# Kernel tuning notes

Hardware: AMD Instinct MI355X
Metric: run time of the kernel (lower is better)

Reference implementation:

```python
import jax, jax.numpy as jnp
import numpy as np

B, L, D = 2, 2048, 1024
H, G = 16, 2            # num_heads, num_kv_groups
HPG = H // G            # heads per kv group = 8
DQK, DV = 128, 128      # qk_head_dim, v_head_dim (head_dim=64, ratios=2.0)


def setup_inputs() -> dict:
    key = jax.random.key(0)
    ks = jax.random.split(key, 12)

    def xavier(k, shape, scale=1.0):
        fan_in, fan_out = shape[0], shape[1]
        lim = np.sqrt(6.0 / (fan_in + fan_out))
        return jax.random.uniform(k, shape, jnp.float32, -lim, lim) * scale

    return {
        "in_q": jax.random.normal(ks[0], (B, L, D), jnp.float32),
        "in_k": jax.random.normal(ks[1], (B, L, D), jnp.float32),
        "in_v": jax.random.normal(ks[2], (B, L, D), jnp.float32),
        # weights stored as [in, out] (transpose of torch Linear); qk_init_scale=0.5
        "Wq": xavier(ks[3], (D, H * DQK), 0.5),
        "bq": jnp.zeros((H * DQK,), jnp.float32),
        "Wk": xavier(ks[4], (D, G * DQK), 0.5),
        "bk": jnp.zeros((G * DQK,), jnp.float32),
        "Wv": xavier(ks[5], (D, G * DV)),
        "bv": jnp.zeros((G * DV,), jnp.float32),
        "Wo": xavier(ks[6], (H * DV, D)),
        "bo": jnp.zeros((D,), jnp.float32),
        "q_extra_scale": jnp.ones((1,), jnp.float32),
    }


def reference(in_q, in_k, in_v, Wq, bq, Wk, bk, Wv, bv, Wo, bo, q_extra_scale):
    # fused projections
    q = (in_q @ Wq + bq) * q_extra_scale              # [B,L,H*DQK]
    k = in_k @ Wk + bk                                 # [B,L,G*DQK]
    v = in_v @ Wv + bv                                 # [B,L,G*DV]

    # reshape: keep GQA group structure instead of materializing repeat_interleave
    q = q.reshape(B, L, G, HPG, DQK)                   # heads grouped: head h = g*HPG + m
    k = k.reshape(B, L, G, DQK)
    v = v.reshape(B, L, G, DV)

    scale = 1.0 / np.sqrt(DQK)
    # scores: [B,G,HPG,L_q,L_kv]
    scores = jnp.einsum("bsgmd,btgd->bgmst", q, k) * scale
    causal = jnp.tril(jnp.ones((L, L), bool))          # is_causal=True
    scores = jnp.where(causal, scores, jnp.finfo(scores.dtype).min)
    attn = jax.nn.softmax(scores, axis=-1)
    ctx = jnp.einsum("bgmst,btgd->bsgmd", attn, v)     # [B,L,G,HPG,DV]
    ctx = ctx.reshape(B, L, H * DV)
    return ctx @ Wo + bo                               # [B,L,D]
```

## Files before the change

### kernel.cpp

```cpp
#include <hip/hip_runtime.h>


typedef __bf16 bf16;
typedef __bf16 bf16x8 __attribute__((ext_vector_type(8)));
typedef __bf16 bf16x4 __attribute__((ext_vector_type(4)));
typedef float f32x4 __attribute__((ext_vector_type(4)));
typedef float f32x16 __attribute__((ext_vector_type(16)));
typedef float float4v __attribute__((ext_vector_type(4)));

#define MFMA_BF16(a, b, c) __builtin_amdgcn_mfma_f32_16x16x32_bf16((a), (b), (c), 0, 0, 0)
#define MFMA32(a, b, c)    __builtin_amdgcn_mfma_f32_32x32x16_bf16((a), (b), (c), 0, 0, 0)

static constexpr int Bz = 2, Lz = 2048, Dz = 1024;
static constexpr int Hz = 16, Gz = 2;
static constexpr int DQKz = 128, DVz = 128;

__device__ __forceinline__ void async_copy16(const bf16* g, bf16* l) {
    __builtin_amdgcn_global_load_lds(
        (const __attribute__((address_space(1))) unsigned int*)g,
        (__attribute__((address_space(3))) unsigned int*)l, 16, 0, 0);
}

__device__ __forceinline__ unsigned cvt_pk_bf16(float lo, float hi) {
    unsigned r;
    asm("v_cvt_pk_bf16_f32 %0, %1, %2" : "=v"(r) : "v"(lo), "v"(hi));
    return r;
}

__global__ __launch_bounds__(256) void prep(
    const float* __restrict__ q, const float* __restrict__ k,
    const float* __restrict__ v, bf16* __restrict__ dq,
    bf16* __restrict__ dk, bf16* __restrict__ dv,
    const float* __restrict__ Wq, const float* __restrict__ Wk,
    const float* __restrict__ Wv, const float* __restrict__ Wo,
    bf16* __restrict__ WqT, bf16* __restrict__ WkT,
    bf16* __restrict__ WvT, bf16* __restrict__ WoT)
{
    int bid = blockIdx.x;
    if (bid < 6144) {
        const float* s = bid < 2048 ? q : (bid < 4096 ? k : v);
        bf16* d = bid < 2048 ? dq : (bid < 4096 ? dk : dv);
        int i = (bid & 2047) * 2048 + threadIdx.x * 8;
        float4v a = *(const float4v*)(s + i);
        float4v b = *(const float4v*)(s + i + 4);
        bf16x8 o;
        #pragma unroll
        for (int j = 0; j < 4; ++j) { o[j] = (bf16)a[j]; o[j + 4] = (bf16)b[j]; }
        *(bf16x8*)(d + i) = o;
        return;
    }
    bid -= 6144;
    const float* W; bf16* WT; int K, N;
    if (bid < 2048)      { W = Wq; WT = WqT; K = 1024; N = 2048; }
    else if (bid < 2304) { W = Wk; WT = WkT; K = 1024; N = 256;  bid -= 2048; }
    else if (bid < 2560) { W = Wv; WT = WvT; K = 1024; N = 256;  bid -= 2304; }
    else                 { W = Wo; WT = WoT; K = 2048; N = 1024; bid -= 2560; }
    int tiles_n = N >> 5;
    int n0 = (bid % tiles_n) * 32, k0 = (bid / tiles_n) * 32;

    __shared__ bf16 t[32][33];
    int tx = threadIdx.x & 31, ty = threadIdx.x >> 5;
    #pragma unroll
    for (int i = 0; i < 4; ++i)
        t[ty + i * 8][tx] = (bf16)W[(size_t)(k0 + ty + i * 8) * N + n0 + tx];
    __syncthreads();
    #pragma unroll
    for (int i = 0; i < 4; ++i)
        WT[(size_t)(n0 + ty + i * 8) * K + k0 + tx] = t[tx][ty + i * 8];
}

template <typename TC>
__device__ __forceinline__ void gemm_tile(
    const bf16* __restrict__ A, const bf16* __restrict__ BT,
    const float* __restrict__ bias, float scale, TC* __restrict__ C,
    int M, int N, int K, int m0, int n0, bool trans_out,
    bf16 (&As)[2][128 * 64], bf16 (&Bs)[2][128 * 64])
{
    const int tid  = threadIdx.x;
    const int wave = tid >> 6;
    const int lane = tid & 63;
    const int quad = lane >> 4;
    const int l16  = lane & 15;
    const int sw   = l16 & 7;
    const int wm = wave >> 2, wn = wave & 3;

    f32x4 acc[4][2] = {};

    auto stage = [&](int k0, int buf) {
        #pragma unroll
        for (int s = 0; s < 2; ++s) {
            int i = s * 512 + tid;
            int row = i >> 3, c = (i & 7) ^ (row & 7);
            async_copy16(A + (size_t)(m0 + row) * K + k0 + c * 8, &As[buf][i * 8]);
        }
        #pragma unroll
        for (int s = 0; s < 2; ++s) {
            int i = s * 512 + tid;
            int row = i >> 3, c = (i & 7) ^ (row & 7);
            async_copy16(BT + (size_t)(n0 + row) * K + k0 + c * 8, &Bs[buf][i * 8]);
        }
    };

    stage(0, 0);
    int cur = 0;
    for (int k0 = 0; k0 < K; k0 += 64) {
        __syncthreads();
        if (k0 + 64 < K) stage(k0 + 64, cur ^ 1);

        #pragma unroll
        for (int ks = 0; ks < 2; ++ks) {
            bf16x8 af[4], bfv[2];
            #pragma unroll
            for (int mt = 0; mt < 4; ++mt)
                af[mt] = *(const bf16x8*)(&As[cur][((wm * 64 + mt * 16 + l16) * 8
                                                    + ((ks * 4 + quad) ^ sw)) * 8]);
            #pragma unroll
            for (int nt = 0; nt < 2; ++nt)
                bfv[nt] = *(const bf16x8*)(&Bs[cur][((wn * 32 + nt * 16 + l16) * 8
                                                     + ((ks * 4 + quad) ^ sw)) * 8]);
            #pragma unroll
            for (int mt = 0; mt < 4; ++mt)
                #pragma unroll
                for (int nt = 0; nt < 2; ++nt)
                    acc[mt][nt] = MFMA_BF16(af[mt], bfv[nt], acc[mt][nt]);
        }
        cur ^= 1;
    }

    #pragma unroll
    for (int nt = 0; nt < 2; ++nt) {
        int col = n0 + wn * 32 + nt * 16 + l16;
        float bv = bias[col];
        #pragma unroll
        for (int mt = 0; mt < 4; ++mt) {
            int row = m0 + wm * 64 + mt * 16 + quad * 4;
            if (trans_out) {
                struct V4 { TC v[4]; } o;
                #pragma unroll
                for (int r = 0; r < 4; ++r)
                    o.v[r] = (TC)((acc[mt][nt][r] + bv) * scale);
                *(V4*)(&C[(size_t)col * M + row]) = o;
            } else {
                #pragma unroll
                for (int r = 0; r < 4; ++r)
                    C[(size_t)(row + r) * N + col] =
                        (TC)((acc[mt][nt][r] + bv) * scale);
            }
        }
    }
}

__global__ __launch_bounds__(512, 4) void proj_qkv(
    const bf16* __restrict__ aq, const bf16* __restrict__ ak,
    const bf16* __restrict__ av, const bf16* __restrict__ WqT,
    const bf16* __restrict__ WkT, const bf16* __restrict__ WvT,
    const float* __restrict__ bq, const float* __restrict__ bk,
    const float* __restrict__ bv, const float* __restrict__ qsc,
    bf16* __restrict__ Qw, bf16* __restrict__ Kw, bf16* __restrict__ VwT)
{
    __shared__ bf16 As[2][128 * 64];
    __shared__ bf16 Bs[2][128 * 64];
    int bid = blockIdx.x;
    if (bid < 512) {
        float scale = qsc[0] * 0.08838834764831845f * 1.4426950408889634f;
        gemm_tile<bf16>(aq, WqT, bq, scale, Qw, 4096, 2048, 1024,
                        (bid >> 4) * 128, (bid & 15) * 128, false, As, Bs);
    } else if (bid < 576) {
        int b2 = bid - 512;
        gemm_tile<bf16>(ak, WkT, bk, 1.0f, Kw, 4096, 256, 1024,
                        (b2 >> 1) * 128, (b2 & 1) * 128, false, As, Bs);
    } else {
        int b2 = bid - 576;
        gemm_tile<bf16>(av, WvT, bv, 1.0f, VwT, 4096, 256, 1024,
                        (b2 >> 1) * 128, (b2 & 1) * 128, true, As, Bs);
    }
}

__global__ __launch_bounds__(512, 4) void proj_o(
    const bf16* __restrict__ Cw, const bf16* __restrict__ WoT,
    const float* __restrict__ bo, float* __restrict__ out)
{
    __shared__ bf16 As[2][128 * 64];
    __shared__ bf16 Bs[2][128 * 64];
    gemm_tile<float>(Cw, WoT, bo, 1.0f, out, 4096, 1024, 2048,
                     (blockIdx.x >> 3) * 128, (blockIdx.x & 7) * 128,
                     false, As, Bs);
}

__global__ __launch_bounds__(256, 2) void attn_fused(
    const bf16* __restrict__ Q,
    const bf16* __restrict__ Kp,
    const bf16* __restrict__ VT,
    bf16* __restrict__ ctx)
{
    __shared__ bf16 Kb[2][64 * 128];
    __shared__ bf16 Vb[2][128 * 64];

    const int tid  = threadIdx.x;
    const int wave = tid >> 6;
    const int lane = tid & 63;
    const int hi   = lane >> 5;
    const int l31  = lane & 31;
    const int s7   = l31 & 7;
    const int wq   = wave >> 1;
    const int kvw  = wave & 1;

    const int h = blockIdx.y;
    const int b = blockIdx.z;
    const int g = h >> 3;

    const bf16* kgbase = Kp + (size_t)(b * Lz) * (Gz * DQKz) + g * DQKz;
    const bf16* vgbase = VT + (size_t)(g * DVz) * (Bz * Lz) + b * Lz;

    int kgo[4], vgo[4], ldso[4];
    #pragma unroll
    for (int s = 0; s < 4; ++s) {
        int i = s * 256 + tid;
        ldso[s] = i * 8;
        int key = i >> 4, ck = (i & 15) ^ (key & 7);
        kgo[s] = key * (Gz * DQKz) + ck * 8;
        int dvr = i >> 3, cv = (i & 7) ^ (dvr & 7);
        vgo[s] = dvr * (Bz * Lz) + cv * 8;
    }
    auto stage = [&](int kt, int buf) {
        const bf16* kb = kgbase + (size_t)(kt * 64) * (Gz * DQKz);
        const bf16* vb = vgbase + kt * 64;
        #pragma unroll
        for (int s = 0; s < 4; ++s) async_copy16(kb + kgo[s], &Kb[buf][ldso[s]]);
        #pragma unroll
        for (int s = 0; s < 4; ++s) async_copy16(vb + vgo[s], &Vb[buf][ldso[s]]);
    };

    int koff[8];
    #pragma unroll
    for (int ks = 0; ks < 8; ++ks)
        koff[ks] = ((kvw * 32 + l31) * 16 + ((ks * 2 + hi) ^ s7)) * 8;
    int voff[4][2];
    #pragma unroll
    for (int dt = 0; dt < 4; ++dt)
        #pragma unroll
        for (int kss = 0; kss < 2; ++kss)
            voff[dt][kss] = ((dt * 32 + l31) * 8
                             + ((kvw * 4 + kss * 2 + hi) ^ s7)) * 8;

    for (int pass = 0; pass < 2; ++pass) {
        const int qt  = pass == 0 ? (31 - (int)blockIdx.x) : (int)blockIdx.x;
        const int q0  = qt * 64;
        const int nkt = qt + 1;
        const int qrow = q0 + wq * 32 + l31;

        bf16x8 qf[8];
        {
            const bf16* qbase = Q + (size_t)(b * Lz + qrow) * (Hz * DQKz) + h * DQKz;
            #pragma unroll
            for (int s = 0; s < 8; ++s)
                qf[s] = *(const bf16x8*)(qbase + s * 16 + hi * 8);
        }

        f32x16 oacc0 = {}, oacc1 = {}, oacc2 = {}, oacc3 = {};
        float lsum = 0.0f;

        if (pass) __syncthreads();
        stage(0, 0);
        int cur = 0;

        for (int kt = 0; kt < nkt; ++kt) {
            __syncthreads();
            if (kt + 1 < nkt) stage(kt + 1, cur ^ 1);

            const bf16* kcur = Kb[cur];
            const bf16* vcur = Vb[cur];

            f32x16 sacc = {};
            #pragma unroll
            for (int ks = 0; ks < 8; ++ks) {
                bf16x8 kf = *(const bf16x8*)(kcur + koff[ks]);
                sacc = MFMA32(kf, qf[ks], sacc);
            }

            float pv[16];
            if (kt == nkt - 1) {
                #pragma unroll
                for (int r = 0; r < 16; ++r) {
                    int key = kvw * 32 + (r & 3) + 8 * (r >> 2) + 4 * hi;
                    pv[r] = (key > wq * 32 + l31) ? 0.0f
                                                  : exp2f(sacc[r] - 8.0f);
                }
            } else {
                #pragma unroll
                for (int r = 0; r < 16; ++r)
                    pv[r] = exp2f(sacc[r] - 8.0f);
            }
            lsum += ((pv[0] + pv[1]) + (pv[2] + pv[3]))
                  + ((pv[4] + pv[5]) + (pv[6] + pv[7]))
                  + ((pv[8] + pv[9]) + (pv[10] + pv[11]))
                  + ((pv[12] + pv[13]) + (pv[14] + pv[15]));

            unsigned c0 = cvt_pk_bf16(pv[0],  pv[1]);
            unsigned c1 = cvt_pk_bf16(pv[2],  pv[3]);
            unsigned c2 = cvt_pk_bf16(pv[4],  pv[5]);
            unsigned c3 = cvt_pk_bf16(pv[6],  pv[7]);
            unsigned c4 = cvt_pk_bf16(pv[8],  pv[9]);
            unsigned c5 = cvt_pk_bf16(pv[10], pv[11]);
            unsigned c6 = cvt_pk_bf16(pv[12], pv[13]);
            unsigned c7 = cvt_pk_bf16(pv[14], pv[15]);
            asm("v_permlane32_swap_b32 %0, %1" : "+v"(c0), "+v"(c2));
            asm("v_permlane32_swap_b32 %0, %1" : "+v"(c1), "+v"(c3));
            asm("v_permlane32_swap_b32 %0, %1" : "+v"(c4), "+v"(c6));
            asm("v_permlane32_swap_b32 %0, %1" : "+v"(c5), "+v"(c7));
            union { unsigned u[4]; bf16x8 v; } p0 = {{c0, c1, c2, c3}};
            union { unsigned u[4]; bf16x8 v; } p1 = {{c4, c5, c6, c7}};

            {
                bf16x8 vf;
                vf = *(const bf16x8*)(vcur + voff[0][0]); oacc0 = MFMA32(vf, p0.v, oacc0);
                vf = *(const bf16x8*)(vcur + voff[0][1]); oacc0 = MFMA32(vf, p1.v, oacc0);
                vf = *(const bf16x8*)(vcur + voff[1][0]); oacc1 = MFMA32(vf, p0.v, oacc1);
                vf = *(const bf16x8*)(vcur + voff[1][1]); oacc1 = MFMA32(vf, p1.v, oacc1);
                vf = *(const bf16x8*)(vcur + voff[2][0]); oacc2 = MFMA32(vf, p0.v, oacc2);
                vf = *(const bf16x8*)(vcur + voff[2][1]); oacc2 = MFMA32(vf, p1.v, oacc2);
                vf = *(const bf16x8*)(vcur + voff[3][0]); oacc3 = MFMA32(vf, p0.v, oacc3);
                vf = *(const bf16x8*)(vcur + voff[3][1]); oacc3 = MFMA32(vf, p1.v, oacc3);
            }
            cur ^= 1;
        }

        lsum += __shfl_xor(lsum, 32);

        float* E0 = (float*)Kb;
        float* E1 = (float*)Vb;
        float* LS = (float*)Vb + 6000;
        __syncthreads();

        auto store_partial = [&](f32x16 v, float* E) {
            #pragma unroll
            for (int j = 0; j < 4; ++j) {
                f32x4 v4 = { v[4 * j], v[4 * j + 1], v[4 * j + 2], v[4 * j + 3] };
                *(f32x4*)&E[(wave * 64 + lane) * 20 + 4 * j] = v4;
            }
        };
        if (kvw == 0) { store_partial(oacc2, E0); store_partial(oacc3, E1); }
        else          { store_partial(oacc0, E0); store_partial(oacc1, E1); }
        if (lane < 32) LS[wave * 32 + lane] = lsum;
        __syncthreads();
        lsum += LS[(wave ^ 1) * 32 + l31];
        const float inv = 1.0f / lsum;

        bf16* cbase = ctx + (size_t)(b * Lz + qrow) * (Hz * DVz) + h * DVz;
        auto finalize = [&](f32x16 v, float* E, int dt) {
            #pragma unroll
            for (int j = 0; j < 4; ++j) {
                f32x4 p4 = *(const f32x4*)&E[((wave ^ 1) * 64 + lane) * 20 + 4 * j];
                bf16x4 o4;
                #pragma unroll
                for (int r = 0; r < 4; ++r)
                    o4[r] = (bf16)((v[4 * j + r] + p4[r]) * inv);
                *(bf16x4*)&cbase[dt * 32 + j * 8 + hi * 4] = o4;
            }
        };
        if (kvw == 0) { finalize(oacc0, E0, 0); finalize(oacc1, E1, 1); }
        else          { finalize(oacc2, E0, 2); finalize(oacc3, E1, 3); }
    }
}

extern "C" void kernel_launch(void* const* d_in, const int* in_sizes, int n_in,
                              void* d_out, int out_size, void* d_ws, size_t ws_size,
                              hipStream_t stream)
{
    (void)in_sizes; (void)n_in; (void)out_size; (void)ws_size;

    const float* in_q = (const float*)d_in[0];
    const float* in_k = (const float*)d_in[1];
    const float* in_v = (const float*)d_in[2];
    const float* Wq   = (const float*)d_in[3];
    const float* bq   = (const float*)d_in[4];
    const float* Wk   = (const float*)d_in[5];
    const float* bk   = (const float*)d_in[6];
    const float* Wv   = (const float*)d_in[7];
    const float* bv   = (const float*)d_in[8];
    const float* Wo   = (const float*)d_in[9];
    const float* bo   = (const float*)d_in[10];
    const float* qsc  = (const float*)d_in[11];
    float* out = (float*)d_out;

    const int M = Bz * Lz;
    const int NQ = Hz * DQKz;
    const int NKV = Gz * DQKz;

    bf16* aq  = (bf16*)d_ws;
    bf16* WqT = aq  + (size_t)M * Dz;
    bf16* WkT = WqT + (size_t)NQ * Dz;
    bf16* WvT = WkT + (size_t)NKV * Dz;
    bf16* WoT = WvT + (size_t)NKV * Dz;
    bf16* Qw  = WoT + (size_t)Dz * NQ;
    bf16* Kw  = Qw  + (size_t)M * NQ;
    bf16* VwT = Kw  + (size_t)M * NKV;
    bf16* Cw  = VwT + (size_t)NKV * M;
    bf16* ak  = Cw;
    bf16* av  = Cw + (size_t)M * Dz;

    prep<<<dim3(10752), dim3(256), 0, stream>>>(
        in_q, in_k, in_v, aq, ak, av, Wq, Wk, Wv, Wo, WqT, WkT, WvT, WoT);

    proj_qkv<<<dim3(640), dim3(512), 0, stream>>>(
        aq, ak, av, WqT, WkT, WvT, bq, bk, bv, qsc, Qw, Kw, VwT);

    attn_fused<<<dim3(Lz / 128, Hz, Bz), dim3(256), 0, stream>>>(Qw, Kw, VwT, Cw);

    proj_o<<<dim3(256), dim3(512), 0, stream>>>(Cw, WoT, bo, out);
}
```

Baseline: 246.0 us.

## Single-buffer K, one q-tile per block, raise attention occupancy

The attention kernel no longer processes two paired q-tiles per block. It launches one block per 64-row q-tile (32 blocks along x) and relies on scheduling to balance the causal work. K is now single-buffered in shared memory while V stays double-buffered, cutting LDS from 64KB to 48KB so three blocks can fit per CU (launch bounds 3). An extra barrier separates the QK MFMAs from the next K/V prefetch, and s_setprio raises wave priority around the MFMA sections. The cost is less K prefetch overlap, since the K load now waits until the QK step finishes, plus one more barrier per iteration and a loss of the explicit load balancing the tile pairing provided.

```diff
diff --git a/kernel.cpp b/kernel.cpp
--- a/kernel.cpp
+++ b/kernel.cpp
@@ -187,14 +187,13 @@
                      false, As, Bs);
 }
 
-__global__ __launch_bounds__(256, 2) void attn_fused(
+__global__ __launch_bounds__(256, 3) void attn_fused(
     const bf16* __restrict__ Q,
     const bf16* __restrict__ Kp,
     const bf16* __restrict__ VT,
     bf16* __restrict__ ctx)
 {
-    __shared__ bf16 Kb[2][64 * 128];
-    __shared__ bf16 Vb[2][128 * 64];
+    __shared__ bf16 smem[24576];
 
     const int tid  = threadIdx.x;
     const int wave = tid >> 6;
@@ -222,13 +221,16 @@
         int dvr = i >> 3, cv = (i & 7) ^ (dvr & 7);
         vgo[s] = dvr * (Bz * Lz) + cv * 8;
     }
-    auto stage = [&](int kt, int buf) {
+    auto stage_K = [&](int kt) {
         const bf16* kb = kgbase + (size_t)(kt * 64) * (Gz * DQKz);
+        #pragma unroll
+        for (int s = 0; s < 4; ++s) async_copy16(kb + kgo[s], smem + ldso[s]);
+    };
+    auto stage_V = [&](int kt, int buf) {
         const bf16* vb = vgbase + kt * 64;
         #pragma unroll
-        for (int s = 0; s < 4; ++s) async_copy16(kb + kgo[s], &Kb[buf][ldso[s]]);
-        #pragma unroll
-        for (int s = 0; s < 4; ++s) async_copy16(vb + vgo[s], &Vb[buf][ldso[s]]);
+        for (int s = 0; s < 4; ++s)
+            async_copy16(vb + vgo[s], smem + 8192 + buf * 8192 + ldso[s]);
     };
 
     int koff[8];
@@ -243,124 +245,131 @@
             voff[dt][kss] = ((dt * 32 + l31) * 8
                              + ((kvw * 4 + kss * 2 + hi) ^ s7)) * 8;
 
-    for (int pass = 0; pass < 2; ++pass) {
-        const int qt  = pass == 0 ? (31 - (int)blockIdx.x) : (int)blockIdx.x;
-        const int q0  = qt * 64;
-        const int nkt = qt + 1;
-        const int qrow = q0 + wq * 32 + l31;
-
-        bf16x8 qf[8];
+    const int qt  = 31 - (int)blockIdx.x;
+    const int q0  = qt * 64;
+    const int nkt = qt + 1;
+    const int qrow = q0 + wq * 32 + l31;
+
+    bf16x8 qf[8];
+    {
+        const bf16* qbase = Q + (size_t)(b * Lz + qrow) * (Hz * DQKz) + h * DQKz;
+        #pragma unroll
+        for (int s = 0; s < 8; ++s)
+            qf[s] = *(const bf16x8*)(qbase + s * 16 + hi * 8);
+    }
+
+    f32x16 oacc0 = {}, oacc1 = {}, oacc2 = {}, oacc3 = {};
+    float lsum = 0.0f;
+
+    stage_K(0);
+    stage_V(0, 0);
+    int cur = 0;
+
+    for (int kt = 0; kt < nkt; ++kt) {
+        __syncthreads();
+
+        const bf16* vcur = smem + 8192 + cur * 8192;
+
+        f32x16 sacc = {};
+        __builtin_amdgcn_s_setprio(1);
+        #pragma unroll
+        for (int ks = 0; ks < 8; ++ks) {
+            bf16x8 kf = *(const bf16x8*)(smem + koff[ks]);
+            sacc = MFMA32(kf, qf[ks], sacc);
+        }
+        __builtin_amdgcn_s_setprio(0);
+
+        __syncthreads();
+        if (kt + 1 < nkt) {
+            stage_K(kt + 1);
+            stage_V(kt + 1, cur ^ 1);
+        }
+
+        float pv[16];
+        if (kt == nkt - 1) {
+            #pragma unroll
+            for (int r = 0; r < 16; ++r) {
+                int key = kvw * 32 + (r & 3) + 8 * (r >> 2) + 4 * hi;
+                pv[r] = (key > wq * 32 + l31) ? 0.0f
+                                              : exp2f(sacc[r] - 8.0f);
+            }
+        } else {
+            #pragma unroll
+            for (int r = 0; r < 16; ++r)
+                pv[r] = exp2f(sacc[r] - 8.0f);
+        }
+        lsum += ((pv[0] + pv[1]) + (pv[2] + pv[3]))
+              + ((pv[4] + pv[5]) + (pv[6] + pv[7]))
+              + ((pv[8] + pv[9]) + (pv[10] + pv[11]))
+              + ((pv[12] + pv[13]) + (pv[14] + pv[15]));
+
+        unsigned c0 = cvt_pk_bf16(pv[0],  pv[1]);
+        unsigned c1 = cvt_pk_bf16(pv[2],  pv[3]);
+        unsigned c2 = cvt_pk_bf16(pv[4],  pv[5]);
+        unsigned c3 = cvt_pk_bf16(pv[6],  pv[7]);
+        unsigned c4 = cvt_pk_bf16(pv[8],  pv[9]);
+        unsigned c5 = cvt_pk_bf16(pv[10], pv[11]);
+        unsigned c6 = cvt_pk_bf16(pv[12], pv[13]);
+        unsigned c7 = cvt_pk_bf16(pv[14], pv[15]);
+        asm("v_permlane32_swap_b32 %0, %1" : "+v"(c0), "+v"(c2));
+        asm("v_permlane32_swap_b32 %0, %1" : "+v"(c1), "+v"(c3));
+        asm("v_permlane32_swap_b32 %0, %1" : "+v"(c4), "+v"(c6));
+        asm("v_permlane32_swap_b32 %0, %1" : "+v"(c5), "+v"(c7));
+        union { unsigned u[4]; bf16x8 v; } p0 = {{c0, c1, c2, c3}};
+        union { unsigned u[4]; bf16x8 v; } p1 = {{c4, c5, c6, c7}};
+
+        __builtin_amdgcn_s_setprio(1);
         {
-            const bf16* qbase = Q + (size_t)(b * Lz + qrow) * (Hz * DQKz) + h * DQKz;
-            #pragma unroll
-            for (int s = 0; s < 8; ++s)
-                qf[s] = *(const bf16x8*)(qbase + s * 16 + hi * 8);
-        }
-
-        f32x16 oacc0 = {}, oacc1 = {}, oacc2 = {}, oacc3 = {};
-        float lsum = 0.0f;
-
-        if (pass) __syncthreads();
-        stage(0, 0);
-        int cur = 0;
-
-        for (int kt = 0; kt < nkt; ++kt) {
-            __syncthreads();
-            if (kt + 1 < nkt) stage(kt + 1, cur ^ 1);
-
-            const bf16* kcur = Kb[cur];
-            const bf16* vcur = Vb[cur];
-
-            f32x16 sacc = {};
-            #pragma unroll
-            for (int ks = 0; ks < 8; ++ks) {
-                bf16x8 kf = *(const bf16x8*)(kcur + koff[ks]);
-                sacc = MFMA32(kf, qf[ks], sacc);
-            }
-
-            float pv[16];
-            if (kt == nkt - 1) {
-                #pragma unroll
-                for (int r = 0; r < 16; ++r) {
-                    int key = kvw * 32 + (r & 3) + 8 * (r >> 2) + 4 * hi;
-                    pv[r] = (key > wq * 32 + l31) ? 0.0f
-                                                  : exp2f(sacc[r] - 8.0f);
-                }
-            } else {
-                #pragma unroll
-                for (int r = 0; r < 16; ++r)
-                    pv[r] = exp2f(sacc[r] - 8.0f);
-            }
-            lsum += ((pv[0] + pv[1]) + (pv[2] + pv[3]))
-                  + ((pv[4] + pv[5]) + (pv[6] + pv[7]))
-                  + ((pv[8] + pv[9]) + (pv[10] + pv[11]))
-                  + ((pv[12] + pv[13]) + (pv[14] + pv[15]));
-
-            unsigned c0 = cvt_pk_bf16(pv[0],  pv[1]);
-            unsigned c1 = cvt_pk_bf16(pv[2],  pv[3]);
-            unsigned c2 = cvt_pk_bf16(pv[4],  pv[5]);
-            unsigned c3 = cvt_pk_bf16(pv[6],  pv[7]);
-            unsigned c4 = cvt_pk_bf16(pv[8],  pv[9]);
-            unsigned c5 = cvt_pk_bf16(pv[10], pv[11]);
-            unsigned c6 = cvt_pk_bf16(pv[12], pv[13]);
-            unsigned c7 = cvt_pk_bf16(pv[14], pv[15]);
-            asm("v_permlane32_swap_b32 %0, %1" : "+v"(c0), "+v"(c2));
-            asm("v_permlane32_swap_b32 %0, %1" : "+v"(c1), "+v"(c3));
-            asm("v_permlane32_swap_b32 %0, %1" : "+v"(c4), "+v"(c6));
-            asm("v_permlane32_swap_b32 %0, %1" : "+v"(c5), "+v"(c7));
-            union { unsigned u[4]; bf16x8 v; } p0 = {{c0, c1, c2, c3}};
-            union { unsigned u[4]; bf16x8 v; } p1 = {{c4, c5, c6, c7}};
-
-            {
-                bf16x8 vf;
-                vf = *(const bf16x8*)(vcur + voff[0][0]); oacc0 = MFMA32(vf, p0.v, oacc0);
-                vf = *(const bf16x8*)(vcur + voff[0][1]); oacc0 = MFMA32(vf, p1.v, oacc0);
-                vf = *(const bf16x8*)(vcur + voff[1][0]); oacc1 = MFMA32(vf, p0.v, oacc1);
-                vf = *(const bf16x8*)(vcur + voff[1][1]); oacc1 = MFMA32(vf, p1.v, oacc1);
-                vf = *(const bf16x8*)(vcur + voff[2][0]); oacc2 = MFMA32(vf, p0.v, oacc2);
-                vf = *(const bf16x8*)(vcur + voff[2][1]); oacc2 = MFMA32(vf, p1.v, oacc2);
-                vf = *(const bf16x8*)(vcur + voff[3][0]); oacc3 = MFMA32(vf, p0.v, oacc3);
-                vf = *(const bf16x8*)(vcur + voff[3][1]); oacc3 = MFMA32(vf, p1.v, oacc3);
-            }
-            cur ^= 1;
-        }
-
-        lsum += __shfl_xor(lsum, 32);
-
-        float* E0 = (float*)Kb;
-        float* E1 = (float*)Vb;
-        float* LS = (float*)Vb + 6000;
-        __syncthreads();
-
-        auto store_partial = [&](f32x16 v, float* E) {
-            #pragma unroll
-            for (int j = 0; j < 4; ++j) {
-                f32x4 v4 = { v[4 * j], v[4 * j + 1], v[4 * j + 2], v[4 * j + 3] };
-                *(f32x4*)&E[(wave * 64 + lane) * 20 + 4 * j] = v4;
-            }
-        };
-        if (kvw == 0) { store_partial(oacc2, E0); store_partial(oacc3, E1); }
-        else          { store_partial(oacc0, E0); store_partial(oacc1, E1); }
-        if (lane < 32) LS[wave * 32 + lane] = lsum;
-        __syncthreads();
-        lsum += LS[(wave ^ 1) * 32 + l31];
-        const float inv = 1.0f / lsum;
-
-        bf16* cbase = ctx + (size_t)(b * Lz + qrow) * (Hz * DVz) + h * DVz;
-        auto finalize = [&](f32x16 v, float* E, int dt) {
-            #pragma unroll
-            for (int j = 0; j < 4; ++j) {
-                f32x4 p4 = *(const f32x4*)&E[((wave ^ 1) * 64 + lane) * 20 + 4 * j];
-                bf16x4 o4;
-                #pragma unroll
-                for (int r = 0; r < 4; ++r)
-                    o4[r] = (bf16)((v[4 * j + r] + p4[r]) * inv);
-                *(bf16x4*)&cbase[dt * 32 + j * 8 + hi * 4] = o4;
-            }
-        };
-        if (kvw == 0) { finalize(oacc0, E0, 0); finalize(oacc1, E1, 1); }
-        else          { finalize(oacc2, E0, 2); finalize(oacc3, E1, 3); }
-    }
+            bf16x8 vf;
+            vf = *(const bf16x8*)(vcur + voff[0][0]); oacc0 = MFMA32(vf, p0.v, oacc0);
+            vf = *(const bf16x8*)(vcur + voff[0][1]); oacc0 = MFMA32(vf, p1.v, oacc0);
+            vf = *(const bf16x8*)(vcur + voff[1][0]); oacc1 = MFMA32(vf, p0.v, oacc1);
+            vf = *(const bf16x8*)(vcur + voff[1][1]); oacc1 = MFMA32(vf, p1.v, oacc1);
+            vf = *(const bf16x8*)(vcur + voff[2][0]); oacc2 = MFMA32(vf, p0.v, oacc2);
+            vf = *(const bf16x8*)(vcur + voff[2][1]); oacc2 = MFMA32(vf, p1.v, oacc2);
+            vf = *(const bf16x8*)(vcur + voff[3][0]); oacc3 = MFMA32(vf, p0.v, oacc3);
+            vf = *(const bf16x8*)(vcur + voff[3][1]); oacc3 = MFMA32(vf, p1.v, oacc3);
+        }
+        __builtin_amdgcn_s_setprio(0);
+        cur ^= 1;
+    }
+
+    lsum += __shfl_xor(lsum, 32);
+
+    float* SM = (float*)smem;
+    float* E0 = SM;
+    float* E1 = SM + 5120;
+    float* LS = SM + 10240;
+    __syncthreads();
+
+    auto store_partial = [&](f32x16 v, float* E) {
+        #pragma unroll
+        for (int j = 0; j < 4; ++j) {
+            f32x4 v4 = { v[4 * j], v[4 * j + 1], v[4 * j + 2], v[4 * j + 3] };
+            *(f32x4*)&E[(wave * 64 + lane) * 20 + 4 * j] = v4;
+        }
+    };
+    if (kvw == 0) { store_partial(oacc2, E0); store_partial(oacc3, E1); }
+    else          { store_partial(oacc0, E0); store_partial(oacc1, E1); }
+    if (lane < 32) LS[wave * 32 + lane] = lsum;
+    __syncthreads();
+    lsum += LS[(wave ^ 1) * 32 + l31];
+    const float inv = 1.0f / lsum;
+
+    bf16* cbase = ctx + (size_t)(b * Lz + qrow) * (Hz * DVz) + h * DVz;
+    auto finalize = [&](f32x16 v, float* E, int dt) {
+        #pragma unroll
+        for (int j = 0; j < 4; ++j) {
+            f32x4 p4 = *(const f32x4*)&E[((wave ^ 1) * 64 + lane) * 20 + 4 * j];
+            bf16x4 o4;
+            #pragma unroll
+            for (int r = 0; r < 4; ++r)
+                o4[r] = (bf16)((v[4 * j + r] + p4[r]) * inv);
+            *(bf16x4*)&cbase[dt * 32 + j * 8 + hi * 4] = o4;
+        }
+    };
+    if (kvw == 0) { finalize(oacc0, E0, 0); finalize(oacc1, E1, 1); }
+    else          { finalize(oacc2, E0, 2); finalize(oacc3, E1, 3); }
 }
 
 extern "C" void kernel_launch(void* const* d_in, const int* in_sizes, int n_in,
@@ -405,7 +414,7 @@
     proj_qkv<<<dim3(640), dim3(512), 0, stream>>>(
         aq, ak, av, WqT, WkT, WvT, bq, bk, bv, qsc, Qw, Kw, VwT);
 
-    attn_fused<<<dim3(Lz / 128, Hz, Bz), dim3(256), 0, stream>>>(Qw, Kw, VwT, Cw);
+    attn_fused<<<dim3(32, Hz, Bz), dim3(256), 0, stream>>>(Qw, Kw, VwT, Cw);
 
     proj_o<<<dim3(256), dim3(512), 0, stream>>>(Cw, WoT, bo, out);
 }
```

New measurement: 281.7 us. +14.5%, slower.
